# Kernel tuning notes

Measured on AMD Instinct MI355X. Metric: run time of the kernel, lower is better.

Reference implementation:

```python
import jax, jax.numpy as jnp
import numpy as np

L, B, H, IN = 4, 256, 1024, 1024

def setup_inputs() -> dict:
    key = jax.random.key(0)
    ks = jax.random.split(key, 7)
    return {
        "x": jax.random.normal(ks[0], (B, IN), jnp.float32),
        "h0": jax.random.normal(ks[1], (L, B, H), jnp.float32),
        "c0": jax.random.normal(ks[2], (L, B, H), jnp.float32),
        "w_ih": jax.random.normal(ks[3], (L, 4 * H, IN), jnp.float32) * 0.02,
        "w_hh": jax.random.normal(ks[4], (L, 4 * H, H), jnp.float32) * 0.02,
        "b_ih": jax.random.normal(ks[5], (L, 4 * H), jnp.float32) * 0.02,
        "b_hh": jax.random.normal(ks[6], (L, 4 * H), jnp.float32) * 0.02,
    }

def _lstm_cell(inp, h, c, wi, wh, bi, bh):
    # gates: (B, 4H), PyTorch gate order i, f, g, o
    gates = jnp.dot(inp, wi.T) + jnp.dot(h, wh.T) + bi + bh
    i_g, f_g, g_g, o_g = jnp.split(gates, 4, axis=-1)
    c_new = jax.nn.sigmoid(f_g) * c + jax.nn.sigmoid(i_g) * jnp.tanh(g_g)
    h_new = jax.nn.sigmoid(o_g) * jnp.tanh(c_new)
    return h_new, c_new

def reference(x, h0, c0, w_ih, w_hh, b_ih, b_hh):
    # Sequential over layers (inter-layer dependency); dropout is identity (eval mode / p=0).
    inp = x
    hs, cs = [], []
    for i in range(h0.shape[0]):
        h, c = _lstm_cell(inp, h0[i], c0[i], w_ih[i], w_hh[i], b_ih[i], b_hh[i])
        hs.append(h)
        cs.append(c)
        inp = h
    return jnp.stack(hs, axis=0), jnp.stack(cs, axis=0)
```

## Files before the change

kernel.cpp:

```cpp
#include <hip/hip_runtime.h>

#define NLAYER 4
#define BATCH  256
#define HID    1024

typedef float f32x4 __attribute__((ext_vector_type(4)));
typedef short short8 __attribute__((ext_vector_type(8)));
typedef unsigned short ushort_t;
typedef unsigned long long u64;

#define BAR()     asm volatile("s_barrier")
#define WAITV(n)  asm volatile("s_waitcnt vmcnt(" #n ")")
#define WAITV_TIE2(n, x, y) \
  asm volatile("s_waitcnt vmcnt(" #n ")" : "+v"(x), "+v"(y))
#define DSR(d, a) asm volatile("ds_read_b128 %0, %1" : "=v"(d) : "v"(a))
#define LGKM0_TIE4(a,b,c,d) \
  asm volatile("s_waitcnt lgkmcnt(0)" : "+v"(a),"+v"(b),"+v"(c),"+v"(d))
#define FULLBAR() asm volatile("s_waitcnt vmcnt(0) lgkmcnt(0)\ns_barrier" ::: "memory")
#define GLD16(d, a) asm volatile("global_load_dwordx4 %0, %1, off" : "=v"(d) : "v"(a))

__device__ __forceinline__ unsigned short f2bf(float f) {
  unsigned int u = __float_as_uint(f);
  unsigned int r = u + 0x7fffu + ((u >> 16) & 1u);
  return (unsigned short)(r >> 16);
}
__device__ __forceinline__ float sigm(float x) { return 1.f / (1.f + __expf(-x)); }
__device__ __forceinline__ float tanh_(float x) { return 2.f / (1.f + __expf(-2.f * x)) - 1.f; }

__device__ __forceinline__ void dma16(const void* g, void* l) {
  __builtin_amdgcn_global_load_lds(
      (const __attribute__((address_space(1))) unsigned int*)g,
      (__attribute__((address_space(3))) unsigned int*)l, 16, 0, 0);
}


__global__ __launch_bounds__(256) void pack_w(const float* __restrict__ w_ih,
                                              const float* __restrict__ w_hh,
                                              ushort_t* __restrict__ wpk) {
  int t   = blockIdx.x * 256 + threadIdx.x;
  int j16 = t & 63;
  int m   = t >> 6;
  int l   = m >> 13;
  int sel = (m >> 12) & 1;
  int row = m & 4095;
  const float* src = (sel ? w_hh : w_ih) + (size_t)l * 4194304
                   + (size_t)row * 1024 + j16 * 16;
  float4 v0 = ((const float4*)src)[0], v1 = ((const float4*)src)[1];
  float4 v2 = ((const float4*)src)[2], v3 = ((const float4*)src)[3];

  int gate = row >> 10, nb = (row & 1023) >> 4, rlow = row & 15;
  int r  = gate * 16 + rlow;
  int g  = r >> 3;
  int kt = sel * 16 + (j16 >> 2);
  int cA = (j16 & 3) * 2;
  int iA = (r & 7) * 8 + ((cA ^ r) & 7);
  int iB = iA ^ 1;
  size_t base = ((size_t)(l * 64 + nb) * 32 + kt) * 4096 + g * 512;

  short8 pA, pB;
  pA[0]=f2bf(v0.x); pA[1]=f2bf(v0.y); pA[2]=f2bf(v0.z); pA[3]=f2bf(v0.w);
  pA[4]=f2bf(v1.x); pA[5]=f2bf(v1.y); pA[6]=f2bf(v1.z); pA[7]=f2bf(v1.w);
  pB[0]=f2bf(v2.x); pB[1]=f2bf(v2.y); pB[2]=f2bf(v2.z); pB[3]=f2bf(v2.w);
  pB[4]=f2bf(v3.x); pB[5]=f2bf(v3.y); pB[6]=f2bf(v3.z); pB[7]=f2bf(v3.w);
  *(short8*)(wpk + base + iA * 8) = pA;
  *(short8*)(wpk + base + iB * 8) = pB;
}

__global__ __launch_bounds__(256) void pack_a(const float* __restrict__ x,
                                              const float* __restrict__ h0,
                                              ushort_t* __restrict__ apk) {
  int t = blockIdx.x * 256 + threadIdx.x;
  int lane = t & 63;
  int r8 = lane >> 3;
  int c = (lane & 7) ^ r8;
  const float* src;
  ushort_t* dst;
  if (t < 32768) {
    int g = (t >> 6) & 7, kt = (t >> 9) & 15, mb = t >> 13;
    int m = mb * 64 + g * 8 + r8;
    src = x + (size_t)m * 1024 + kt * 64 + c * 8;
    dst = apk + (size_t)mb * 131072 + (size_t)kt * 4096 + g * 512 + lane * 8;
  } else {
    int u = t - 32768;
    int g = (u >> 6) & 7, kt16 = (u >> 9) & 15, mb = (u >> 13) & 3, l = u >> 15;
    int m = mb * 64 + g * 8 + r8;
    src = h0 + (size_t)l * 262144 + (size_t)m * 1024 + kt16 * 64 + c * 8;
    dst = apk + (size_t)l * 524288 + (size_t)mb * 131072
        + (size_t)(16 + kt16) * 4096 + g * 512 + lane * 8;
  }
  float4 a = *(const float4*)src, b = *(const float4*)(src + 4);
  short8 pk;
  pk[0] = (short)f2bf(a.x); pk[1] = (short)f2bf(a.y);
  pk[2] = (short)f2bf(a.z); pk[3] = (short)f2bf(a.w);
  pk[4] = (short)f2bf(b.x); pk[5] = (short)f2bf(b.y);
  pk[6] = (short)f2bf(b.z); pk[7] = (short)f2bf(b.w);
  *(short8*)dst = pk;
}

__global__ __launch_bounds__(512) void lstm_fused(
    const ushort_t* __restrict__ apk, const ushort_t* __restrict__ wpk,
    const float* __restrict__ bi, const float* __restrict__ bh,
    const float* __restrict__ c0l,
    float* __restrict__ hout, float* __restrict__ cout,
    ushort_t* __restrict__ apk_next) {
  __shared__ union U {
    ushort_t stage[4][4096];
    float sg[4 * 64 * 17];
  } sm;

  const int tid = threadIdx.x;
  const int nb = blockIdx.x;
  const int mb = blockIdx.y;
  const int h0c = nb * 16;
  const int m0 = mb * 64;
  const int lane = tid & 63;
  const int w = tid >> 6;
  const int wm = w & 3, wcol = w >> 2;
  const int lrow = lane & 15, lq = lane >> 4;

  const char* srcB = (const char*)(wpk + (size_t)nb * 131072 + w * 512 + lane * 8);

  const int rA = wm * 16 + lrow;
#define CHUNK(r, c) (((r) >> 3) * 64 + ((r) & 7) * 8 + (((c) ^ (r)) & 7))
  u64 aA0 = (u64)(const char*)(apk + (size_t)mb * 131072 + CHUNK(rA, lq) * 8);
  u64 aA1 = (u64)(const char*)(apk + (size_t)mb * 131072 + CHUNK(rA, 4 + lq) * 8);

  unsigned smb = (unsigned)(uintptr_t)(__attribute__((address_space(3))) void*)&sm;
  const int rB0 = wcol * 32 + lrow, rB1 = rB0 + 16;
  unsigned oB00 = smb + CHUNK(rB0, lq) * 16, oB01 = smb + CHUNK(rB0, 4 + lq) * 16;
  unsigned oB10 = smb + CHUNK(rB1, lq) * 16, oB11 = smb + CHUNK(rB1, 4 + lq) * 16;
#undef CHUNK

  f32x4 acc0 = {0.f, 0.f, 0.f, 0.f}, acc1 = {0.f, 0.f, 0.f, 0.f};
  short8 areg[4][2];

#pragma unroll
  for (int t = 0; t < 3; ++t) {
    dma16(srcB, &sm.stage[t][w * 512]);
    srcB += 8192;
    GLD16(areg[t][0], aA0); aA0 += 8192;
    GLD16(areg[t][1], aA1); aA1 += 8192;
  }

#define KSTEP(S, PRE, POST, ISSUE)                                          \
  {                                                                         \
    WAITV(PRE);                                                             \
    BAR();                                                                  \
    if (ISSUE) {                                                            \
      dma16(srcB, &sm.stage[(S + 3) & 3][w * 512]);                         \
      srcB += 8192;                                                         \
      GLD16(areg[(S + 3) & 3][0], aA0); aA0 += 8192;                        \
      GLD16(areg[(S + 3) & 3][1], aA1); aA1 += 8192;                        \
    }                                                                       \
    WAITV_TIE2(POST, areg[S][0], areg[S][1]);                               \
    short8 b00, b01, b10, b11;                                              \
    DSR(b00, oB00 + (S) * 8192u); DSR(b10, oB10 + (S) * 8192u);             \
    DSR(b01, oB01 + (S) * 8192u); DSR(b11, oB11 + (S) * 8192u);             \
    LGKM0_TIE4(b00, b01, b10, b11);                                         \
    acc0 = __builtin_amdgcn_mfma_f32_16x16x32_bf16(areg[S][0], b00, acc0, 0, 0, 0); \
    acc1 = __builtin_amdgcn_mfma_f32_16x16x32_bf16(areg[S][0], b10, acc1, 0, 0, 0); \
    acc0 = __builtin_amdgcn_mfma_f32_16x16x32_bf16(areg[S][1], b01, acc0, 0, 0, 0); \
    acc1 = __builtin_amdgcn_mfma_f32_16x16x32_bf16(areg[S][1], b11, acc1, 0, 0, 0); \
  }

  for (int i = 0; i < 7; ++i) {
    KSTEP(0, 8, 9, 1)
    KSTEP(1, 8, 9, 1)
    KSTEP(2, 8, 9, 1)
    KSTEP(3, 8, 9, 1)
  }
  KSTEP(0, 8, 9, 1)
  KSTEP(1, 8, 6, 0)
  KSTEP(2, 5, 3, 0)
  KSTEP(3, 2, 0, 0)
#undef KSTEP

  FULLBAR();

#pragma unroll
  for (int nt = 0; nt < 2; ++nt) {
    int gate = wcol * 2 + nt;
    int rowb = wm * 16 + lq * 4;
    const f32x4& a = nt ? acc1 : acc0;
#pragma unroll
    for (int r = 0; r < 4; ++r)
      sm.sg[gate * 1088 + (rowb + r) * 17 + lrow] = a[r];
  }
  FULLBAR();

  {
    const int erow = tid >> 3, ehp = (tid & 7) * 2;
    float2 cp = *(const float2*)(c0l + (size_t)(m0 + erow) * 1024 + h0c + ehp);
    float cpa[2] = {cp.x, cp.y};
    float hva[2], cva[2];
#pragma unroll
    for (int e = 0; e < 2; ++e) {
      int hc = ehp + e;
      float gi = sm.sg[0 * 1088 + erow * 17 + hc] + bi[h0c + hc]          + bh[h0c + hc];
      float gf = sm.sg[1 * 1088 + erow * 17 + hc] + bi[1024 + h0c + hc]   + bh[1024 + h0c + hc];
      float gg = sm.sg[2 * 1088 + erow * 17 + hc] + bi[2048 + h0c + hc]   + bh[2048 + h0c + hc];
      float go = sm.sg[3 * 1088 + erow * 17 + hc] + bi[3072 + h0c + hc]   + bh[3072 + h0c + hc];
      float cn = sigm(gf) * cpa[e] + sigm(gi) * tanh_(gg);
      cva[e] = cn;
      hva[e] = sigm(go) * tanh_(cn);
    }
    float2 hv; hv.x = hva[0]; hv.y = hva[1];
    float2 cv; cv.x = cva[0]; cv.y = cva[1];
    *(float2*)(hout + (size_t)(m0 + erow) * 1024 + h0c + ehp) = hv;
    *(float2*)(cout + (size_t)(m0 + erow) * 1024 + h0c + ehp) = cv;
    if (apk_next) {
      int g = erow >> 3;
#pragma unroll
      for (int e = 0; e < 2; ++e) {
        int k = h0c + ehp + e;
        int cc = (k >> 3) & 7, j = k & 7;
        int i = (erow & 7) * 8 + ((cc ^ erow) & 7);
        apk_next[(size_t)mb * 131072 + (size_t)(k >> 6) * 4096 + g * 512 + i * 8 + j] =
            f2bf(hva[e]);
      }
    }
  }
}

extern "C" void kernel_launch(void* const* d_in, const int* in_sizes, int n_in,
                              void* d_out, int out_size, void* d_ws, size_t ws_size,
                              hipStream_t stream) {
  const float* x    = (const float*)d_in[0];
  const float* h0   = (const float*)d_in[1];
  const float* c0   = (const float*)d_in[2];
  const float* w_ih = (const float*)d_in[3];
  const float* w_hh = (const float*)d_in[4];
  const float* b_ih = (const float*)d_in[5];
  const float* b_hh = (const float*)d_in[6];
  float* out = (float*)d_out;

  ushort_t* Wpk = (ushort_t*)d_ws;
  ushort_t* Apk = Wpk + (size_t)4 * 8388608;

  pack_w<<<8192, 256, 0, stream>>>(w_ih, w_hh, Wpk);
  pack_a<<<640, 256, 0, stream>>>(x, h0, Apk);

  const size_t BH = (size_t)BATCH * HID;
  for (int l = 0; l < NLAYER; ++l) {
    lstm_fused<<<dim3(64, 4), 512, 0, stream>>>(
        Apk + (size_t)l * 524288, Wpk + (size_t)l * 8388608,
        b_ih + (size_t)l * 4096, b_hh + (size_t)l * 4096,
        c0 + (size_t)l * BH,
        out + (size_t)l * BH, out + (size_t)NLAYER * BH + (size_t)l * BH,
        (l < NLAYER - 1) ? Apk + (size_t)(l + 1) * 524288 : (ushort_t*)nullptr);
  }
}
```

Measured before the change: 221.3 us.

## Fuse weight bf16 conversion into LSTM GEMM, dropping separate pack_w pass

Removes the pack_w kernel that converted fp32 weights to a swizzled bf16 workspace and instead loads fp32 weight rows directly in lstm_fused, converting to bf16 in registers and writing them to LDS with ds_write. This avoids one full read+write pass over the 128 MB of weights plus a kernel launch. In exchange each GEMM block reads fp32 weights (twice the bytes of bf16), the pipeline now needs a register conversion step and an extra LDS wait/barrier per k-step, and register pressure rises from the fp32 staging buffers.

```diff
diff --git a/kernel.cpp b/kernel.cpp
--- a/kernel.cpp
+++ b/kernel.cpp
@@ -10,14 +10,21 @@
 typedef unsigned long long u64;
 
 #define BAR()     asm volatile("s_barrier")
-#define WAITV(n)  asm volatile("s_waitcnt vmcnt(" #n ")")
 #define WAITV_TIE2(n, x, y) \
   asm volatile("s_waitcnt vmcnt(" #n ")" : "+v"(x), "+v"(y))
+#define WAITV_TIE4(n, x, y, z, u) \
+  asm volatile("s_waitcnt vmcnt(" #n ")" : "+v"(x), "+v"(y), "+v"(z), "+v"(u))
 #define DSR(d, a) asm volatile("ds_read_b128 %0, %1" : "=v"(d) : "v"(a))
+#define DSW(a, d) asm volatile("ds_write_b128 %0, %1" :: "v"(a), "v"(d))
+#define LGKM0()   asm volatile("s_waitcnt lgkmcnt(0)")
 #define LGKM0_TIE4(a,b,c,d) \
   asm volatile("s_waitcnt lgkmcnt(0)" : "+v"(a),"+v"(b),"+v"(c),"+v"(d))
 #define FULLBAR() asm volatile("s_waitcnt vmcnt(0) lgkmcnt(0)\ns_barrier" ::: "memory")
 #define GLD16(d, a) asm volatile("global_load_dwordx4 %0, %1, off" : "=v"(d) : "v"(a))
+#define GLDB(d0, d1, a) asm volatile( \
+    "global_load_dwordx4 %0, %2, off\n\t" \
+    "global_load_dwordx4 %1, %2, off offset:16" \
+    : "=&v"(d0), "=&v"(d1) : "v"(a))
 
 __device__ __forceinline__ unsigned short f2bf(float f) {
   unsigned int u = __float_as_uint(f);
@@ -27,44 +34,15 @@
 __device__ __forceinline__ float sigm(float x) { return 1.f / (1.f + __expf(-x)); }
 __device__ __forceinline__ float tanh_(float x) { return 2.f / (1.f + __expf(-2.f * x)) - 1.f; }
 
-__device__ __forceinline__ void dma16(const void* g, void* l) {
-  __builtin_amdgcn_global_load_lds(
-      (const __attribute__((address_space(1))) unsigned int*)g,
-      (__attribute__((address_space(3))) unsigned int*)l, 16, 0, 0);
-}
-
-
-__global__ __launch_bounds__(256) void pack_w(const float* __restrict__ w_ih,
-                                              const float* __restrict__ w_hh,
-                                              ushort_t* __restrict__ wpk) {
-  int t   = blockIdx.x * 256 + threadIdx.x;
-  int j16 = t & 63;
-  int m   = t >> 6;
-  int l   = m >> 13;
-  int sel = (m >> 12) & 1;
-  int row = m & 4095;
-  const float* src = (sel ? w_hh : w_ih) + (size_t)l * 4194304
-                   + (size_t)row * 1024 + j16 * 16;
-  float4 v0 = ((const float4*)src)[0], v1 = ((const float4*)src)[1];
-  float4 v2 = ((const float4*)src)[2], v3 = ((const float4*)src)[3];
-
-  int gate = row >> 10, nb = (row & 1023) >> 4, rlow = row & 15;
-  int r  = gate * 16 + rlow;
-  int g  = r >> 3;
-  int kt = sel * 16 + (j16 >> 2);
-  int cA = (j16 & 3) * 2;
-  int iA = (r & 7) * 8 + ((cA ^ r) & 7);
-  int iB = iA ^ 1;
-  size_t base = ((size_t)(l * 64 + nb) * 32 + kt) * 4096 + g * 512;
-
-  short8 pA, pB;
-  pA[0]=f2bf(v0.x); pA[1]=f2bf(v0.y); pA[2]=f2bf(v0.z); pA[3]=f2bf(v0.w);
-  pA[4]=f2bf(v1.x); pA[5]=f2bf(v1.y); pA[6]=f2bf(v1.z); pA[7]=f2bf(v1.w);
-  pB[0]=f2bf(v2.x); pB[1]=f2bf(v2.y); pB[2]=f2bf(v2.z); pB[3]=f2bf(v2.w);
-  pB[4]=f2bf(v3.x); pB[5]=f2bf(v3.y); pB[6]=f2bf(v3.z); pB[7]=f2bf(v3.w);
-  *(short8*)(wpk + base + iA * 8) = pA;
-  *(short8*)(wpk + base + iB * 8) = pB;
-}
+__device__ __forceinline__ short8 cvt8(f32x4 a, f32x4 b) {
+  short8 p;
+  p[0] = (short)f2bf(a[0]); p[1] = (short)f2bf(a[1]);
+  p[2] = (short)f2bf(a[2]); p[3] = (short)f2bf(a[3]);
+  p[4] = (short)f2bf(b[0]); p[5] = (short)f2bf(b[1]);
+  p[6] = (short)f2bf(b[2]); p[7] = (short)f2bf(b[3]);
+  return p;
+}
+
 
 __global__ __launch_bounds__(256) void pack_a(const float* __restrict__ x,
                                               const float* __restrict__ h0,
@@ -98,7 +76,8 @@
 }
 
 __global__ __launch_bounds__(512) void lstm_fused(
-    const ushort_t* __restrict__ apk, const ushort_t* __restrict__ wpk,
+    const ushort_t* __restrict__ apk,
+    const float* __restrict__ wih, const float* __restrict__ whh,
     const float* __restrict__ bi, const float* __restrict__ bh,
     const float* __restrict__ c0l,
     float* __restrict__ hout, float* __restrict__ cout,
@@ -118,14 +97,19 @@
   const int wm = w & 3, wcol = w >> 2;
   const int lrow = lane & 15, lq = lane >> 4;
 
-  const char* srcB = (const char*)(wpk + (size_t)nb * 131072 + w * 512 + lane * 8);
-
+#define CHUNK(r, c) (((r) >> 3) * 64 + ((r) & 7) * 8 + (((c) ^ (r)) & 7))
   const int rA = wm * 16 + lrow;
-#define CHUNK(r, c) (((r) >> 3) * 64 + ((r) & 7) * 8 + (((c) ^ (r)) & 7))
   u64 aA0 = (u64)(const char*)(apk + (size_t)mb * 131072 + CHUNK(rA, lq) * 8);
   u64 aA1 = (u64)(const char*)(apk + (size_t)mb * 131072 + CHUNK(rA, 4 + lq) * 8);
 
+  const int rW = tid >> 3, cW = tid & 7;
+  const int gate = rW >> 4;
+  const size_t wroff = (size_t)(gate * 1024 + nb * 16 + (rW & 15)) * 1024 + cW * 8;
+  u64 aB  = (u64)(const char*)(wih + wroff);
+  u64 hhA = (u64)(const char*)(whh + wroff);
+
   unsigned smb = (unsigned)(uintptr_t)(__attribute__((address_space(3))) void*)&sm;
+  unsigned dsw = smb + CHUNK(rW, cW) * 16;
   const int rB0 = wcol * 32 + lrow, rB1 = rB0 + 16;
   unsigned oB00 = smb + CHUNK(rB0, lq) * 16, oB01 = smb + CHUNK(rB0, 4 + lq) * 16;
   unsigned oB10 = smb + CHUNK(rB1, lq) * 16, oB11 = smb + CHUNK(rB1, 4 + lq) * 16;
@@ -133,26 +117,40 @@
 
   f32x4 acc0 = {0.f, 0.f, 0.f, 0.f}, acc1 = {0.f, 0.f, 0.f, 0.f};
   short8 areg[4][2];
+  f32x4 breg[4][2];
+  int tIss = 3;
 
 #pragma unroll
   for (int t = 0; t < 3; ++t) {
-    dma16(srcB, &sm.stage[t][w * 512]);
-    srcB += 8192;
+    GLDB(breg[t][0], breg[t][1], aB); aB += 256;
     GLD16(areg[t][0], aA0); aA0 += 8192;
     GLD16(areg[t][1], aA1); aA1 += 8192;
   }
-
-#define KSTEP(S, PRE, POST, ISSUE)                                          \
+  WAITV_TIE2(10, breg[0][0], breg[0][1]);
+  {
+    short8 p0 = cvt8(breg[0][0], breg[0][1]);
+    DSW(dsw, p0);
+  }
+  LGKM0();
+  BAR();
+
+#define KSTEP(S, PRE, ISSUE, CONV)                                          \
   {                                                                         \
-    WAITV(PRE);                                                             \
+    const int S1 = ((S) + 1) & 3, S3 = ((S) + 3) & 3;                       \
+    WAITV_TIE4(PRE, breg[S1][0], breg[S1][1], areg[S][0], areg[S][1]);      \
+    if (ISSUE) {                                                            \
+      GLDB(breg[S3][0], breg[S3][1], aB);                                   \
+      ++tIss;                                                               \
+      aB = (tIss == 16) ? hhA : (aB + 256);    \
+      GLD16(areg[S3][0], aA0); aA0 += 8192;                                 \
+      GLD16(areg[S3][1], aA1); aA1 += 8192;                                 \
+    }                                                                       \
+    if (CONV) {                                                             \
+      short8 pk_ = cvt8(breg[S1][0], breg[S1][1]);                          \
+      DSW(dsw + (unsigned)(S1) * 8192u, pk_);                               \
+    }                                                                       \
+    LGKM0();                                                                \
     BAR();                                                                  \
-    if (ISSUE) {                                                            \
-      dma16(srcB, &sm.stage[(S + 3) & 3][w * 512]);                         \
-      srcB += 8192;                                                         \
-      GLD16(areg[(S + 3) & 3][0], aA0); aA0 += 8192;                        \
-      GLD16(areg[(S + 3) & 3][1], aA1); aA1 += 8192;                        \
-    }                                                                       \
-    WAITV_TIE2(POST, areg[S][0], areg[S][1]);                               \
     short8 b00, b01, b10, b11;                                              \
     DSR(b00, oB00 + (S) * 8192u); DSR(b10, oB10 + (S) * 8192u);             \
     DSR(b01, oB01 + (S) * 8192u); DSR(b11, oB11 + (S) * 8192u);             \
@@ -164,27 +162,27 @@
   }
 
   for (int i = 0; i < 7; ++i) {
-    KSTEP(0, 8, 9, 1)
-    KSTEP(1, 8, 9, 1)
-    KSTEP(2, 8, 9, 1)
-    KSTEP(3, 8, 9, 1)
-  }
-  KSTEP(0, 8, 9, 1)
-  KSTEP(1, 8, 6, 0)
-  KSTEP(2, 5, 3, 0)
-  KSTEP(3, 2, 0, 0)
+    KSTEP(0, 6, 1, 1)
+    KSTEP(1, 6, 1, 1)
+    KSTEP(2, 6, 1, 1)
+    KSTEP(3, 6, 1, 1)
+  }
+  KSTEP(0, 6, 1, 1)
+  KSTEP(1, 6, 0, 1)
+  KSTEP(2, 2, 0, 1)
+  KSTEP(3, 0, 0, 0)
 #undef KSTEP
 
   FULLBAR();
 
 #pragma unroll
   for (int nt = 0; nt < 2; ++nt) {
-    int gate = wcol * 2 + nt;
+    int gatee = wcol * 2 + nt;
     int rowb = wm * 16 + lq * 4;
     const f32x4& a = nt ? acc1 : acc0;
 #pragma unroll
     for (int r = 0; r < 4; ++r)
-      sm.sg[gate * 1088 + (rowb + r) * 17 + lrow] = a[r];
+      sm.sg[gatee * 1088 + (rowb + r) * 17 + lrow] = a[r];
   }
   FULLBAR();
 
@@ -234,16 +232,15 @@
   const float* b_hh = (const float*)d_in[6];
   float* out = (float*)d_out;
 
-  ushort_t* Wpk = (ushort_t*)d_ws;
-  ushort_t* Apk = Wpk + (size_t)4 * 8388608;
-
-  pack_w<<<8192, 256, 0, stream>>>(w_ih, w_hh, Wpk);
+  ushort_t* Apk = (ushort_t*)d_ws;
+
   pack_a<<<640, 256, 0, stream>>>(x, h0, Apk);
 
   const size_t BH = (size_t)BATCH * HID;
   for (int l = 0; l < NLAYER; ++l) {
     lstm_fused<<<dim3(64, 4), 512, 0, stream>>>(
-        Apk + (size_t)l * 524288, Wpk + (size_t)l * 8388608,
+        Apk + (size_t)l * 524288,
+        w_ih + (size_t)l * 4194304, w_hh + (size_t)l * 4194304,
         b_ih + (size_t)l * 4096, b_hh + (size_t)l * 4096,
         c0 + (size_t)l * BH,
         out + (size_t)l * BH, out + (size_t)NLAYER * BH + (size_t)l * BH,
```

New measurement: 221.4 us. Within noise of the previous version (+0.1%).

## Overlap next-layer weight packing with current LSTM layer compute

Applied to the files above, without the earlier changes.

Only layer 0's weights are now packed up front, together with the activation pack in one merged kernel. Each layer's LSTM launch gets an extra grid row of blocks that converts and swizzles the next layer's fp32 weights to bf16 while the compute blocks run. The aim is to hide most of the weight-conversion traffic behind the layer GEMMs and drop one launch. The cost is that the packing blocks compete with the compute blocks for HBM bandwidth and CU slots.

```diff
diff --git a/kernel.cpp b/kernel.cpp
--- a/kernel.cpp
+++ b/kernel.cpp
@@ -34,42 +34,36 @@
 }
 
 
-__global__ __launch_bounds__(256) void pack_w(const float* __restrict__ w_ih,
-                                              const float* __restrict__ w_hh,
-                                              ushort_t* __restrict__ wpk) {
-  int t   = blockIdx.x * 256 + threadIdx.x;
-  int j16 = t & 63;
-  int m   = t >> 6;
-  int l   = m >> 13;
-  int sel = (m >> 12) & 1;
-  int row = m & 4095;
-  const float* src = (sel ? w_hh : w_ih) + (size_t)l * 4194304
-                   + (size_t)row * 1024 + j16 * 16;
+__device__ __forceinline__ void pack_chunks(const float* __restrict__ win,
+                                            const float* __restrict__ whn,
+                                            ushort_t* __restrict__ dst,
+                                            int q) {
+  int i = q & 63, g = (q >> 6) & 7, kt = (q >> 9) & 31, nbq = q >> 14;
+  int r = g * 8 + (i >> 3);
+  int c = (i & 7) ^ (r & 7);
+  const float* src = ((kt >> 4) ? whn : win)
+      + ((size_t)((r >> 4) * 1024 + nbq * 16 + (r & 15)) << 10)
+      + ((kt & 15) * 64 + c * 8);
   float4 v0 = ((const float4*)src)[0], v1 = ((const float4*)src)[1];
-  float4 v2 = ((const float4*)src)[2], v3 = ((const float4*)src)[3];
-
-  int gate = row >> 10, nb = (row & 1023) >> 4, rlow = row & 15;
-  int r  = gate * 16 + rlow;
-  int g  = r >> 3;
-  int kt = sel * 16 + (j16 >> 2);
-  int cA = (j16 & 3) * 2;
-  int iA = (r & 7) * 8 + ((cA ^ r) & 7);
-  int iB = iA ^ 1;
-  size_t base = ((size_t)(l * 64 + nb) * 32 + kt) * 4096 + g * 512;
-
-  short8 pA, pB;
-  pA[0]=f2bf(v0.x); pA[1]=f2bf(v0.y); pA[2]=f2bf(v0.z); pA[3]=f2bf(v0.w);
-  pA[4]=f2bf(v1.x); pA[5]=f2bf(v1.y); pA[6]=f2bf(v1.z); pA[7]=f2bf(v1.w);
-  pB[0]=f2bf(v2.x); pB[1]=f2bf(v2.y); pB[2]=f2bf(v2.z); pB[3]=f2bf(v2.w);
-  pB[4]=f2bf(v3.x); pB[5]=f2bf(v3.y); pB[6]=f2bf(v3.z); pB[7]=f2bf(v3.w);
-  *(short8*)(wpk + base + iA * 8) = pA;
-  *(short8*)(wpk + base + iB * 8) = pB;
-}
-
-__global__ __launch_bounds__(256) void pack_a(const float* __restrict__ x,
-                                              const float* __restrict__ h0,
-                                              ushort_t* __restrict__ apk) {
-  int t = blockIdx.x * 256 + threadIdx.x;
+  short8 pk;
+  pk[0] = (short)f2bf(v0.x); pk[1] = (short)f2bf(v0.y);
+  pk[2] = (short)f2bf(v0.z); pk[3] = (short)f2bf(v0.w);
+  pk[4] = (short)f2bf(v1.x); pk[5] = (short)f2bf(v1.y);
+  pk[6] = (short)f2bf(v1.z); pk[7] = (short)f2bf(v1.w);
+  *(short8*)(dst + (size_t)q * 8) = pk;
+}
+
+__global__ __launch_bounds__(256) void pack_init(
+    const float* __restrict__ x, const float* __restrict__ h0,
+    const float* __restrict__ w_ih, const float* __restrict__ w_hh,
+    ushort_t* __restrict__ wpk, ushort_t* __restrict__ apk) {
+  int blk = blockIdx.x;
+  if (blk >= 640) {
+    int q = (blk - 640) * 256 + threadIdx.x;
+    pack_chunks(w_ih, w_hh, wpk, q);
+    return;
+  }
+  int t = blk * 256 + threadIdx.x;
   int lane = t & 63;
   int r8 = lane >> 3;
   int c = (lane & 7) ^ r8;
@@ -102,13 +96,26 @@
     const float* __restrict__ bi, const float* __restrict__ bh,
     const float* __restrict__ c0l,
     float* __restrict__ hout, float* __restrict__ cout,
-    ushort_t* __restrict__ apk_next) {
+    ushort_t* __restrict__ apk_next,
+    const float* __restrict__ win, const float* __restrict__ whn,
+    ushort_t* __restrict__ wpk_next) {
   __shared__ union U {
     ushort_t stage[4][4096];
     float sg[4 * 64 * 17];
   } sm;
 
   const int tid = threadIdx.x;
+
+  if (blockIdx.y == 4) {
+    if (wpk_next) {
+      int t0 = blockIdx.x * 512 + tid;
+#pragma unroll 4
+      for (int k = 0; k < 32; ++k)
+        pack_chunks(win, whn, wpk_next, t0 + k * 32768);
+    }
+    return;
+  }
+
   const int nb = blockIdx.x;
   const int mb = blockIdx.y;
   const int h0c = nb * 16;
@@ -237,16 +244,19 @@
   ushort_t* Wpk = (ushort_t*)d_ws;
   ushort_t* Apk = Wpk + (size_t)4 * 8388608;
 
-  pack_w<<<8192, 256, 0, stream>>>(w_ih, w_hh, Wpk);
-  pack_a<<<640, 256, 0, stream>>>(x, h0, Apk);
+  pack_init<<<4736, 256, 0, stream>>>(x, h0, w_ih, w_hh, Wpk, Apk);
 
   const size_t BH = (size_t)BATCH * HID;
   for (int l = 0; l < NLAYER; ++l) {
-    lstm_fused<<<dim3(64, 4), 512, 0, stream>>>(
+    int nl = l + 1;
+    lstm_fused<<<dim3(64, 5), 512, 0, stream>>>(
         Apk + (size_t)l * 524288, Wpk + (size_t)l * 8388608,
         b_ih + (size_t)l * 4096, b_hh + (size_t)l * 4096,
         c0 + (size_t)l * BH,
         out + (size_t)l * BH, out + (size_t)NLAYER * BH + (size_t)l * BH,
-        (l < NLAYER - 1) ? Apk + (size_t)(l + 1) * 524288 : (ushort_t*)nullptr);
-  }
-}
+        (l < NLAYER - 1) ? Apk + (size_t)nl * 524288 : (ushort_t*)nullptr,
+        w_ih + (size_t)(l < NLAYER - 1 ? nl : 0) * 4194304,
+        w_hh + (size_t)(l < NLAYER - 1 ? nl : 0) * 4194304,
+        (l < NLAYER - 1) ? Wpk + (size_t)nl * 8388608 : (ushort_t*)nullptr);
+  }
+}
```

Result: slower. 269.1 us (+21.6%).
